# Optimization experiments

Measured on AMD Instinct MI355X. Metric: run time of the kernel, lower is better.

Reference implementation:

```python
import jax, jax.numpy as jnp
import numpy as np

N_NODES = 50000
N_EDGES = 800000
NEG_SLOPE = 0.2  # PyG GATConv default negative_slope


def setup_inputs() -> dict:
    key = jax.random.key(0)
    ks = jax.random.split(key, 10)
    d_in, hid, heads = 128, 32, 8

    def glorot(k, shape):
        fan_in, fan_out = shape[0], shape[-1]
        s = jnp.sqrt(2.0 / (fan_in + fan_out)).astype(jnp.float32)
        return jax.random.normal(k, shape, jnp.float32) * s

    return {
        "x": jax.random.normal(ks[0], (N_NODES, d_in), jnp.float32),
        "edge_index": jax.random.randint(ks[1], (2, N_EDGES), 0, N_NODES),
        "W1": glorot(ks[2], (d_in, heads * hid)),
        "a1_src": glorot(ks[3], (heads, hid)),
        "a1_dst": glorot(ks[4], (heads, hid)),
        "b1": jnp.zeros((heads * hid,), jnp.float32),
        "W2": glorot(ks[5], (heads * hid, hid)),
        "a2_src": glorot(ks[6], (1, hid)),
        "a2_dst": glorot(ks[7], (1, hid)),
        "b2": jnp.zeros((hid,), jnp.float32),
    }


def _gat_layer(x, src, dst, W, a_src, a_dst, b, concat):
    # PyG GATConv: h = x @ W, split into heads; alpha_e = softmax_over_dst(
    #   leaky_relu(<h[src], a_src> + <h[dst], a_dst>)); out = scatter-sum alpha*h[src].
    N = x.shape[0]
    H, D = a_src.shape
    h = (x @ W).reshape(N, H, D)                      # [N, H, D]
    score_s = jnp.einsum("nhd,hd->nh", h, a_src)      # [N, H]
    score_d = jnp.einsum("nhd,hd->nh", h, a_dst)
    e = jax.nn.leaky_relu(score_s[src] + score_d[dst], NEG_SLOPE)  # [E, H]
    # numerically-stable softmax over incoming edges per destination node
    m = jax.ops.segment_max(e, dst, num_segments=N)
    ex = jnp.exp(e - m[dst])
    denom = jax.ops.segment_sum(ex, dst, num_segments=N)
    alpha = ex / (denom[dst] + 1e-16)                 # [E, H]
    out = jax.ops.segment_sum(alpha[:, :, None] * h[src], dst, num_segments=N)  # [N, H, D]
    out = out.reshape(N, H * D) if concat else out[:, 0]
    return out + b


def reference(x, edge_index, W1, a1_src, a1_dst, b1, W2, a2_src, a2_dst, b2):
    N = x.shape[0]
    # PyG GATConv add_self_loops=True
    loop = jnp.arange(N, dtype=edge_index.dtype)
    src = jnp.concatenate([edge_index[0], loop])
    dst = jnp.concatenate([edge_index[1], loop])
    h = _gat_layer(x, src, dst, W1, a1_src, a1_dst, b1, concat=True)
    h = jax.nn.relu(h)
    # dropout(p=0.4) is identity in eval mode (deterministic reference)
    return _gat_layer(h, src, dst, W2, a2_src, a2_dst, b2, concat=False)
```

## Files before the change

### kernel.cpp

```cpp
#include <hip/hip_runtime.h>
#include <hip/hip_fp16.h>
#include <math.h>

#define N_NODES 50000
#define N_EDGES 800000
#define E_TOT (N_EDGES + N_NODES)
#define N_RT 3125
#define CAP 64

typedef unsigned int uint;
typedef unsigned short ushort;
typedef float f32x4 __attribute__((ext_vector_type(4)));
typedef short v8s __attribute__((ext_vector_type(8)));

__device__ __forceinline__ ushort f2bf(float f) {
    uint u = __float_as_uint(f);
    return (ushort)((u + 0x7FFFu + ((u >> 16) & 1u)) >> 16);
}
__device__ __forceinline__ float bf2f(ushort u) {
    return __uint_as_float((uint)u << 16);
}
__device__ __forceinline__ float bflo(uint v) { return __uint_as_float(v << 16); }
__device__ __forceinline__ float bfhi(uint v) { return __uint_as_float(v & 0xFFFF0000u); }

__device__ __forceinline__ int kmap(int g, int j) {
    return ((j >> 2) << 4) + (g << 2) + (j & 3);
}


__global__ void wprep_k(const float* __restrict__ W1, const float* __restrict__ a1s,
                        const float* __restrict__ a1d, const float* __restrict__ W2,
                        ushort* __restrict__ W1f, ushort* __restrict__ W2b,
                        ushort* __restrict__ W2r, ushort* __restrict__ Abf,
                        ushort* __restrict__ Arf, int* __restrict__ cnt) {
    for (int i = blockIdx.x * 256 + threadIdx.x; i < N_NODES; i += 21 * 256)
        cnt[i] = 0;

    if (blockIdx.x < 16) {
        int idx = blockIdx.x * 256 + threadIdx.x;
        int lane = idx & 63, ks = (idx >> 6) & 3, ct = idx >> 8;
        int g = lane >> 4, col = ct * 16 + (lane & 15);
        ushort us[8];
        #pragma unroll
        for (int j = 0; j < 8; j++) {
            int k = ks * 32 + kmap(g, j);
            us[j] = f2bf(W1[(size_t)k * 256 + col]);
        }
        uint4 pk;
        pk.x = (uint)us[0] | ((uint)us[1] << 16);
        pk.y = (uint)us[2] | ((uint)us[3] << 16);
        pk.z = (uint)us[4] | ((uint)us[5] << 16);
        pk.w = (uint)us[6] | ((uint)us[7] << 16);
        *((uint4*)(W1f + ((size_t)(ct * 4 + ks) * 64 + lane) * 8)) = pk;
    } else if (blockIdx.x < 20) {
        int idx = (blockIdx.x - 16) * 256 + threadIdx.x;
        int lane = idx & 63, ks = (idx >> 6) & 7, ct = idx >> 9;
        int g = lane >> 4, col = ct * 16 + (lane & 15);
        ushort ub[8], ur[8];
        #pragma unroll
        for (int j = 0; j < 8; j++) {
            int k = ks * 32 + kmap(g, j);
            float v = W2[(size_t)k * 32 + col];
            ub[j] = f2bf(v);
            ur[j] = f2bf(v - bf2f(ub[j]));
        }
        uint4 pb, pr;
        pb.x = (uint)ub[0] | ((uint)ub[1] << 16);
        pb.y = (uint)ub[2] | ((uint)ub[3] << 16);
        pb.z = (uint)ub[4] | ((uint)ub[5] << 16);
        pb.w = (uint)ub[6] | ((uint)ub[7] << 16);
        pr.x = (uint)ur[0] | ((uint)ur[1] << 16);
        pr.y = (uint)ur[2] | ((uint)ur[3] << 16);
        pr.z = (uint)ur[4] | ((uint)ur[5] << 16);
        pr.w = (uint)ur[6] | ((uint)ur[7] << 16);
        *((uint4*)(W2b + ((size_t)(ct * 8 + ks) * 64 + lane) * 8)) = pb;
        *((uint4*)(W2r + ((size_t)(ct * 8 + ks) * 64 + lane) * 8)) = pr;
    } else if (blockIdx.x == 20) {
        int t = threadIdx.x;
        int lane = t & 63, ks = t >> 6;
        int jcol = lane & 15, g = lane >> 4;
        int hh = (jcol < 8) ? jcol : jcol - 8;
        const float* a = (jcol < 8) ? (a1s + hh * 32) : (a1d + hh * 32);
        ushort ub[8], ur[8];
        #pragma unroll
        for (int j = 0; j < 8; j++) {
            int k = ks * 32 + kmap(g, j);
            const float* wrow = W1 + (size_t)k * 256 + hh * 32;
            float v = 0.f;
            #pragma unroll 8
            for (int d = 0; d < 32; d++) v = fmaf(wrow[d], a[d], v);
            ub[j] = f2bf(v);
            ur[j] = f2bf(v - bf2f(ub[j]));
        }
        uint4 pb, pr;
        pb.x = (uint)ub[0] | ((uint)ub[1] << 16);
        pb.y = (uint)ub[2] | ((uint)ub[3] << 16);
        pb.z = (uint)ub[4] | ((uint)ub[5] << 16);
        pb.w = (uint)ub[6] | ((uint)ub[7] << 16);
        pr.x = (uint)ur[0] | ((uint)ur[1] << 16);
        pr.y = (uint)ur[2] | ((uint)ur[3] << 16);
        pr.z = (uint)ur[4] | ((uint)ur[5] << 16);
        pr.w = (uint)ur[6] | ((uint)ur[7] << 16);
        *((uint4*)(Abf + ((size_t)ks * 64 + lane) * 8)) = pb;
        *((uint4*)(Arf + ((size_t)ks * 64 + lane) * 8)) = pr;
    }
}


__global__ __launch_bounds__(256) void scat_k(const int* __restrict__ ei,
                                              int* __restrict__ cnt,
                                              ushort* __restrict__ csr) {
    int t = blockIdx.x * 256 + threadIdx.x;
    if (t < N_EDGES / 8) {
        int4 sv0 = ((const int4*)ei)[2 * t];
        int4 sv1 = ((const int4*)ei)[2 * t + 1];
        int4 dv0 = ((const int4*)(ei + N_EDGES))[2 * t];
        int4 dv1 = ((const int4*)(ei + N_EDGES))[2 * t + 1];
        int p0 = atomicAdd(&cnt[dv0.x], 1);
        int p1 = atomicAdd(&cnt[dv0.y], 1);
        int p2 = atomicAdd(&cnt[dv0.z], 1);
        int p3 = atomicAdd(&cnt[dv0.w], 1);
        int p4 = atomicAdd(&cnt[dv1.x], 1);
        int p5 = atomicAdd(&cnt[dv1.y], 1);
        int p6 = atomicAdd(&cnt[dv1.z], 1);
        int p7 = atomicAdd(&cnt[dv1.w], 1);
        if (p0 < CAP) csr[dv0.x * CAP + p0] = (ushort)sv0.x;
        if (p1 < CAP) csr[dv0.y * CAP + p1] = (ushort)sv0.y;
        if (p2 < CAP) csr[dv0.z * CAP + p2] = (ushort)sv0.z;
        if (p3 < CAP) csr[dv0.w * CAP + p3] = (ushort)sv0.w;
        if (p4 < CAP) csr[dv1.x * CAP + p4] = (ushort)sv1.x;
        if (p5 < CAP) csr[dv1.y * CAP + p5] = (ushort)sv1.y;
        if (p6 < CAP) csr[dv1.z * CAP + p6] = (ushort)sv1.z;
        if (p7 < CAP) csr[dv1.w * CAP + p7] = (ushort)sv1.w;
    } else if (t < N_EDGES / 8 + (N_NODES + 3) / 4) {
        int n0 = (t - N_EDGES / 8) * 4;
        int p[4];
        #pragma unroll
        for (int j = 0; j < 4; j++) {
            int n = n0 + j;
            p[j] = (n < N_NODES) ? atomicAdd(&cnt[n], 1) : CAP;
        }
        #pragma unroll
        for (int j = 0; j < 4; j++) {
            int n = n0 + j;
            if (n < N_NODES && p[j] < CAP) csr[n * CAP + p[j]] = (ushort)n;
        }
    }
}


__global__ __launch_bounds__(256) void fgemm1_k(
        const float* __restrict__ x, const ushort* __restrict__ W1f,
        const ushort* __restrict__ Abf, const ushort* __restrict__ Arf,
        ushort* __restrict__ h1u, float* __restrict__ s1s,
        float* __restrict__ s1d) {
    int lane = threadIdx.x & 63, wv = threadIdx.x >> 6;
    int rt = blockIdx.x * 2 + (wv >> 1);
    int half = wv & 1;
    if (rt >= N_RT) return;
    int r = lane & 15, g = lane >> 4;
    const float* xrow = x + ((size_t)rt * 16 + r) * 128;

    v8s xb[4], xr[4];
    #pragma unroll
    for (int ks = 0; ks < 4; ks++) {
        float4 fa = *((const float4*)(xrow + ks * 32 + g * 4));
        float4 fb = *((const float4*)(xrow + ks * 32 + 16 + g * 4));
        ushort b0 = f2bf(fa.x), b1 = f2bf(fa.y), b2 = f2bf(fa.z), b3 = f2bf(fa.w);
        ushort b4 = f2bf(fb.x), b5 = f2bf(fb.y), b6 = f2bf(fb.z), b7 = f2bf(fb.w);
        uint4 p;
        p.x = (uint)b0 | ((uint)b1 << 16);
        p.y = (uint)b2 | ((uint)b3 << 16);
        p.z = (uint)b4 | ((uint)b5 << 16);
        p.w = (uint)b6 | ((uint)b7 << 16);
        xb[ks] = *((v8s*)&p);
        if (half == 0) {
            ushort r0 = f2bf(fa.x - bf2f(b0)), r1 = f2bf(fa.y - bf2f(b1));
            ushort r2 = f2bf(fa.z - bf2f(b2)), r3 = f2bf(fa.w - bf2f(b3));
            ushort r4 = f2bf(fb.x - bf2f(b4)), r5 = f2bf(fb.y - bf2f(b5));
            ushort r6 = f2bf(fb.z - bf2f(b6)), r7 = f2bf(fb.w - bf2f(b7));
            uint4 q;
            q.x = (uint)r0 | ((uint)r1 << 16);
            q.y = (uint)r2 | ((uint)r3 << 16);
            q.z = (uint)r4 | ((uint)r5 << 16);
            q.w = (uint)r6 | ((uint)r7 << 16);
            xr[ks] = *((v8s*)&q);
        }
    }

    if (half == 0) {
        f32x4 sacc = (f32x4){0.f, 0.f, 0.f, 0.f};
        const v8s* abp = (const v8s*)Abf;
        const v8s* arp = (const v8s*)Arf;
        #pragma unroll
        for (int ks = 0; ks < 4; ks++) {
            v8s ab = abp[ks * 64 + lane];
            v8s ar = arp[ks * 64 + lane];
            sacc = __builtin_amdgcn_mfma_f32_16x16x32_bf16(ab, xb[ks], sacc, 0, 0, 0);
            sacc = __builtin_amdgcn_mfma_f32_16x16x32_bf16(ar, xb[ks], sacc, 0, 0, 0);
            sacc = __builtin_amdgcn_mfma_f32_16x16x32_bf16(ab, xr[ks], sacc, 0, 0, 0);
        }
        int row = rt * 16 + r;
        float4 sv;
        sv.x = sacc[0]; sv.y = sacc[1]; sv.z = sacc[2]; sv.w = sacc[3];
        if (g < 2) *((float4*)(s1s + (size_t)row * 8 + g * 4)) = sv;
        else       *((float4*)(s1d + (size_t)row * 8 + (g - 2) * 4)) = sv;
    }

    f32x4 acc[8];
    #pragma unroll
    for (int c = 0; c < 8; c++) acc[c] = (f32x4){0.f, 0.f, 0.f, 0.f};
    const v8s* bp = (const v8s*)W1f + (size_t)half * 8 * 4 * 64;
    #pragma unroll
    for (int ks = 0; ks < 4; ks++) {
        #pragma unroll
        for (int c = 0; c < 8; c++) {
            v8s wf = bp[(c * 4 + ks) * 64 + lane];
            acc[c] = __builtin_amdgcn_mfma_f32_16x16x32_bf16(wf, xb[ks], acc[c], 0, 0, 0);
        }
    }

    ushort* hrow = h1u + ((size_t)rt * 16 + r) * 256 + half * 128;
    #pragma unroll
    for (int c = 0; c < 8; c++) {
        uint lo = (uint)f2bf(acc[c][0]) | ((uint)f2bf(acc[c][1]) << 16);
        uint hi = (uint)f2bf(acc[c][2]) | ((uint)f2bf(acc[c][3]) << 16);
        *((uint2*)(hrow + c * 16 + g * 4)) = make_uint2(lo, hi);
    }
}


__global__ __launch_bounds__(256) void agg1g_k(
        const ushort* __restrict__ csr, const int* __restrict__ cnt,
        const ushort* __restrict__ h1u, const float* __restrict__ s1s,
        const float* __restrict__ s1d, const float* __restrict__ b1,
        const ushort* __restrict__ W2b, const ushort* __restrict__ W2r,
        const float* __restrict__ a2s, const float* __restrict__ a2d,
        ushort* __restrict__ h2u, float* __restrict__ s2s,
        float* __restrict__ s2d) {
    __shared__ float els[4][CAP][8];
    __shared__ ushort hrt[16][264];
    int lane = threadIdx.x & 63;
    int wv = threadIdx.x >> 6;
    int base = blockIdx.x * 16;
    int e8 = lane >> 3, h8 = lane & 7;
    int hB = lane >> 3;
    int c0 = 4 * lane;
    float4 bv = *((const float4*)(b1 + c0));
    const uint2* hv = (const uint2*)h1u;

    for (int q = 0; q < 4; q++) {
        int row = wv * 4 + q;
        int n = base + row;
        int beg = n * CAP;
        int deg = min(cnt[n], CAP);
        int end = beg + deg;

        float sd = s1d[n * 8 + h8];
        float m = -3.4e38f, d = 0.f;
        for (int i = beg + e8; i < end; i += 8) {
            int s = csr[i];
            float e = s1s[s * 8 + h8] + sd;
            e = (e >= 0.f) ? e : 0.2f * e;
            els[wv][i - beg][h8] = e;
            float mn = fmaxf(m, e);
            d = d * __expf(m - mn) + __expf(e - mn);
            m = mn;
        }
        #pragma unroll
        for (int mask = 8; mask <= 32; mask <<= 1) {
            float om = __shfl_xor(m, mask);
            float od = __shfl_xor(d, mask);
            float nm = fmaxf(m, om);
            d = d * __expf(m - nm) + od * __expf(om - nm);
            m = nm;
        }
        float inv = 1.f / (d + 1e-16f);
        float mB = __shfl(m, hB);
        float invB = __shfl(inv, hB);

        const float* ep = &els[wv][0][hB];
        float acc0 = 0.f, acc1 = 0.f, acc2 = 0.f, acc3 = 0.f;
        int j = 0;
        for (; j + 3 < deg; j += 4) {
            uint2 cs = *((const uint2*)(csr + beg + j));
            int s0 = cs.x & 0xFFFF, s1 = cs.x >> 16;
            int s2 = cs.y & 0xFFFF, s3 = cs.y >> 16;
            float p0 = __expf(ep[(j + 0) * 8] - mB);
            float p1 = __expf(ep[(j + 1) * 8] - mB);
            float p2 = __expf(ep[(j + 2) * 8] - mB);
            float p3 = __expf(ep[(j + 3) * 8] - mB);
            uint2 v0 = hv[(size_t)s0 * 64 + lane];
            uint2 v1 = hv[(size_t)s1 * 64 + lane];
            uint2 v2 = hv[(size_t)s2 * 64 + lane];
            uint2 v3 = hv[(size_t)s3 * 64 + lane];
            acc0 = fmaf(p0, bflo(v0.x), acc0);
            acc1 = fmaf(p0, bfhi(v0.x), acc1);
            acc2 = fmaf(p0, bflo(v0.y), acc2);
            acc3 = fmaf(p0, bfhi(v0.y), acc3);
            acc0 = fmaf(p1, bflo(v1.x), acc0);
            acc1 = fmaf(p1, bfhi(v1.x), acc1);
            acc2 = fmaf(p1, bflo(v1.y), acc2);
            acc3 = fmaf(p1, bfhi(v1.y), acc3);
            acc0 = fmaf(p2, bflo(v2.x), acc0);
            acc1 = fmaf(p2, bfhi(v2.x), acc1);
            acc2 = fmaf(p2, bflo(v2.y), acc2);
            acc3 = fmaf(p2, bfhi(v2.y), acc3);
            acc0 = fmaf(p3, bflo(v3.x), acc0);
            acc1 = fmaf(p3, bfhi(v3.x), acc1);
            acc2 = fmaf(p3, bflo(v3.y), acc2);
            acc3 = fmaf(p3, bfhi(v3.y), acc3);
        }
        for (; j < deg; j++) {
            int s0 = csr[beg + j];
            float p0 = __expf(ep[j * 8] - mB);
            uint2 v0 = hv[(size_t)s0 * 64 + lane];
            acc0 = fmaf(p0, bflo(v0.x), acc0);
            acc1 = fmaf(p0, bfhi(v0.x), acc1);
            acc2 = fmaf(p0, bflo(v0.y), acc2);
            acc3 = fmaf(p0, bfhi(v0.y), acc3);
        }
        float o0 = fmaxf(fmaf(acc0, invB, bv.x), 0.f);
        float o1 = fmaxf(fmaf(acc1, invB, bv.y), 0.f);
        float o2 = fmaxf(fmaf(acc2, invB, bv.z), 0.f);
        float o3 = fmaxf(fmaf(acc3, invB, bv.w), 0.f);
        uint lo = (uint)f2bf(o0) | ((uint)f2bf(o1) << 16);
        uint hi = (uint)f2bf(o2) | ((uint)f2bf(o3) << 16);
        *((uint2*)&hrt[row][c0]) = make_uint2(lo, hi);
    }
    __syncthreads();

    if (threadIdx.x < 64) {
        int r = lane & 15, g = lane >> 4;
        int row = base + r;
        v8s af[8];
        #pragma unroll
        for (int ks = 0; ks < 8; ks++) {
            uint2 u0 = *((const uint2*)&hrt[r][ks * 32 + g * 4]);
            uint2 u1 = *((const uint2*)&hrt[r][ks * 32 + 16 + g * 4]);
            uint4 p; p.x = u0.x; p.y = u0.y; p.z = u1.x; p.w = u1.y;
            af[ks] = *((v8s*)&p);
        }
        f32x4 acc[2];
        acc[0] = (f32x4){0.f, 0.f, 0.f, 0.f};
        acc[1] = (f32x4){0.f, 0.f, 0.f, 0.f};
        const v8s* wbp = (const v8s*)W2b;
        const v8s* wrp = (const v8s*)W2r;
        #pragma unroll
        for (int ks = 0; ks < 8; ks++) {
            #pragma unroll
            for (int ct = 0; ct < 2; ct++) {
                v8s wb = wbp[(ct * 8 + ks) * 64 + lane];
                v8s wr = wrp[(ct * 8 + ks) * 64 + lane];
                acc[ct] = __builtin_amdgcn_mfma_f32_16x16x32_bf16(wb, af[ks], acc[ct], 0, 0, 0);
                acc[ct] = __builtin_amdgcn_mfma_f32_16x16x32_bf16(wr, af[ks], acc[ct], 0, 0, 0);
            }
        }
        float ps = 0.f, pd = 0.f;
        #pragma unroll
        for (int ct = 0; ct < 2; ct++) {
            #pragma unroll
            for (int qq = 0; qq < 4; qq++) {
                int c = ct * 16 + g * 4 + qq;
                ps = fmaf(acc[ct][qq], a2s[c], ps);
                pd = fmaf(acc[ct][qq], a2d[c], pd);
            }
        }
        ps += __shfl_xor(ps, 16); ps += __shfl_xor(ps, 32);
        pd += __shfl_xor(pd, 16); pd += __shfl_xor(pd, 32);
        if (g == 0) { s2s[row] = ps; s2d[row] = pd; }
        #pragma unroll
        for (int ct = 0; ct < 2; ct++) {
            uint lo = (uint)f2bf(acc[ct][0]) | ((uint)f2bf(acc[ct][1]) << 16);
            uint hi = (uint)f2bf(acc[ct][2]) | ((uint)f2bf(acc[ct][3]) << 16);
            *((uint2*)(h2u + (size_t)row * 32 + ct * 16 + g * 4)) = make_uint2(lo, hi);
        }
    }
}


__global__ __launch_bounds__(256) void agg2_k(
        const ushort* __restrict__ csr, const int* __restrict__ cnt,
        const ushort* __restrict__ h2u, const float* __restrict__ s2s,
        const float* __restrict__ s2d, const float* __restrict__ b2,
        float* __restrict__ out) {
    int lane = threadIdx.x & 63;
    int n = blockIdx.x * 4 + (threadIdx.x >> 6);
    int beg = n * CAP;
    int end = beg + min(cnt[n], CAP);
    float sd = s2d[n];

    float m = -3.4e38f, dd = 0.f;
    for (int i = beg + lane; i < end; i += 64) {
        float e = s2s[csr[i]] + sd;
        e = (e >= 0.f) ? e : 0.2f * e;
        float mn = fmaxf(m, e);
        dd = dd * __expf(m - mn) + __expf(e - mn);
        m = mn;
    }
    #pragma unroll
    for (int mask = 1; mask <= 32; mask <<= 1) {
        float om = __shfl_xor(m, mask);
        float od = __shfl_xor(dd, mask);
        float nm = fmaxf(m, om);
        dd = dd * __expf(m - nm) + od * __expf(om - nm);
        m = nm;
    }
    float inv = 1.f / (dd + 1e-16f);

    int e4 = lane >> 4, cp = lane & 15;
    float acc0 = 0.f, acc1 = 0.f;
    for (int c0 = beg; c0 < end; c0 += 64) {
        int i = c0 + lane;
        int sL = 0; float aL = 0.f;
        if (i < end) {
            sL = csr[i];
            float e = s2s[sL] + sd;
            e = (e >= 0.f) ? e : 0.2f * e;
            aL = __expf(e - m) * inv;
        }
        int nsub = min(64, end - c0);
        for (int el = 0; el < nsub; el += 4) {
            int local = el + e4;
            int se = __shfl(sL, local);
            float ae = __shfl(aL, local);
            uint v = *((const uint*)(h2u + (size_t)se * 32 + cp * 2));
            acc0 = fmaf(ae, bflo(v), acc0);
            acc1 = fmaf(ae, bfhi(v), acc1);
        }
    }
    acc0 += __shfl_xor(acc0, 16); acc0 += __shfl_xor(acc0, 32);
    acc1 += __shfl_xor(acc1, 16); acc1 += __shfl_xor(acc1, 32);
    if (lane < 16) {
        float2 bv = ((const float2*)b2)[cp];
        float2 o; o.x = acc0 + bv.x; o.y = acc1 + bv.y;
        ((float2*)(out + (size_t)n * 32))[cp] = o;
    }
}


extern "C" void kernel_launch(void* const* d_in, const int* in_sizes, int n_in,
                              void* d_out, int out_size, void* d_ws, size_t ws_size,
                              hipStream_t stream) {
    const float* x   = (const float*)d_in[0];
    const int*   ei  = (const int*)d_in[1];
    const float* W1  = (const float*)d_in[2];
    const float* a1s = (const float*)d_in[3];
    const float* a1d = (const float*)d_in[4];
    const float* b1  = (const float*)d_in[5];
    const float* W2  = (const float*)d_in[6];
    const float* a2s = (const float*)d_in[7];
    const float* a2d = (const float*)d_in[8];
    const float* b2  = (const float*)d_in[9];
    float* out = (float*)d_out;

    char* w = (char*)d_ws;
    ushort* h1u   = (ushort*)w; w += (size_t)N_NODES * 256 * 2;
    ushort* W1f   = (ushort*)w; w += (size_t)16 * 4 * 64 * 8 * 2;
    ushort* Abf   = (ushort*)w; w += (size_t)4 * 64 * 8 * 2;
    ushort* Arf   = (ushort*)w; w += (size_t)4 * 64 * 8 * 2;
    ushort* W2b   = (ushort*)w; w += (size_t)2 * 8 * 64 * 8 * 2;
    ushort* W2r   = (ushort*)w; w += (size_t)2 * 8 * 64 * 8 * 2;
    ushort* h2u   = (ushort*)w; w += (size_t)N_NODES * 32 * 2;
    float* s1s    = (float*)w;  w += (size_t)N_NODES * 8 * 4;
    float* s1d    = (float*)w;  w += (size_t)N_NODES * 8 * 4;
    float* s2s    = (float*)w;  w += (size_t)N_NODES * 4;
    float* s2d    = (float*)w;  w += (size_t)N_NODES * 4;
    int* cnt    = (int*)w; w += (size_t)N_NODES * 4;
    ushort* csr = (ushort*)w; w += (size_t)N_NODES * CAP * 2;

    int nscat = (N_EDGES / 8 + (N_NODES + 3) / 4 + 255) / 256;

    wprep_k<<<21, 256, 0, stream>>>(W1, a1s, a1d, W2, W1f, W2b, W2r, Abf, Arf, cnt);
    scat_k<<<nscat, 256, 0, stream>>>(ei, cnt, csr);
    fgemm1_k<<<(N_RT + 1) / 2, 256, 0, stream>>>(x, W1f, Abf, Arf, h1u, s1s, s1d);
    agg1g_k<<<N_NODES / 16, 256, 0, stream>>>(csr, cnt, h1u, s1s, s1d, b1,
                                              W2b, W2r, a2s, a2d, h2u, s2s, s2d);
    agg2_k<<<N_NODES / 4, 256, 0, stream>>>(csr, cnt, h2u, s2s, s2d, b2, out);
}
```

Measured before the change: 192.1 us.

## Fuse edge scatter and first-layer GEMM into one launch; pre-seed self loops

Merges the CSR scatter kernel and the layer-1 GEMM kernel into a single launch whose blocks split by index: the first blocks scatter edges and the rest compute the GEMM tiles. The two jobs are independent, so they can overlap on the GPU, and one launch boundary disappears. Self loops are now written in the weight-prep kernel by setting each count to 1 and storing the node's own index in slot 0, so the scatter no longer does atomics for them. Self loops now always sit first in each neighbour list, which changes the summation order slightly but is otherwise equivalent.

```diff
diff --git a/kernel.cpp b/kernel.cpp
--- a/kernel.cpp
+++ b/kernel.cpp
@@ -7,6 +7,7 @@
 #define E_TOT (N_EDGES + N_NODES)
 #define N_RT 3125
 #define CAP 64
+#define NBLK_SCAT ((N_EDGES / 8 + 255) / 256)
 
 typedef unsigned int uint;
 typedef unsigned short ushort;
@@ -32,9 +33,12 @@
                         const float* __restrict__ a1d, const float* __restrict__ W2,
                         ushort* __restrict__ W1f, ushort* __restrict__ W2b,
                         ushort* __restrict__ W2r, ushort* __restrict__ Abf,
-                        ushort* __restrict__ Arf, int* __restrict__ cnt) {
-    for (int i = blockIdx.x * 256 + threadIdx.x; i < N_NODES; i += 21 * 256)
-        cnt[i] = 0;
+                        ushort* __restrict__ Arf, int* __restrict__ cnt,
+                        ushort* __restrict__ csr) {
+    for (int i = blockIdx.x * 256 + threadIdx.x; i < N_NODES; i += 21 * 256) {
+        cnt[i] = 1;
+        csr[(size_t)i * CAP] = (ushort)i;
+    }
 
     if (blockIdx.x < 16) {
         int idx = blockIdx.x * 256 + threadIdx.x;
@@ -107,11 +111,16 @@
 }
 
 
-__global__ __launch_bounds__(256) void scat_k(const int* __restrict__ ei,
-                                              int* __restrict__ cnt,
-                                              ushort* __restrict__ csr) {
-    int t = blockIdx.x * 256 + threadIdx.x;
-    if (t < N_EDGES / 8) {
+__global__ __launch_bounds__(256) void fsg_k(
+        const int* __restrict__ ei, int* __restrict__ cnt,
+        ushort* __restrict__ csr,
+        const float* __restrict__ x, const ushort* __restrict__ W1f,
+        const ushort* __restrict__ Abf, const ushort* __restrict__ Arf,
+        ushort* __restrict__ h1u, float* __restrict__ s1s,
+        float* __restrict__ s1d) {
+    if (blockIdx.x < NBLK_SCAT) {
+        int t = blockIdx.x * 256 + threadIdx.x;
+        if (t >= N_EDGES / 8) return;
         int4 sv0 = ((const int4*)ei)[2 * t];
         int4 sv1 = ((const int4*)ei)[2 * t + 1];
         int4 dv0 = ((const int4*)(ei + N_EDGES))[2 * t];
@@ -132,30 +141,11 @@
         if (p5 < CAP) csr[dv1.y * CAP + p5] = (ushort)sv1.y;
         if (p6 < CAP) csr[dv1.z * CAP + p6] = (ushort)sv1.z;
         if (p7 < CAP) csr[dv1.w * CAP + p7] = (ushort)sv1.w;
-    } else if (t < N_EDGES / 8 + (N_NODES + 3) / 4) {
-        int n0 = (t - N_EDGES / 8) * 4;
-        int p[4];
-        #pragma unroll
-        for (int j = 0; j < 4; j++) {
-            int n = n0 + j;
-            p[j] = (n < N_NODES) ? atomicAdd(&cnt[n], 1) : CAP;
-        }
-        #pragma unroll
-        for (int j = 0; j < 4; j++) {
-            int n = n0 + j;
-            if (n < N_NODES && p[j] < CAP) csr[n * CAP + p[j]] = (ushort)n;
-        }
-    }
-}
-
-
-__global__ __launch_bounds__(256) void fgemm1_k(
-        const float* __restrict__ x, const ushort* __restrict__ W1f,
-        const ushort* __restrict__ Abf, const ushort* __restrict__ Arf,
-        ushort* __restrict__ h1u, float* __restrict__ s1s,
-        float* __restrict__ s1d) {
+        return;
+    }
+
     int lane = threadIdx.x & 63, wv = threadIdx.x >> 6;
-    int rt = blockIdx.x * 2 + (wv >> 1);
+    int rt = (blockIdx.x - NBLK_SCAT) * 2 + (wv >> 1);
     int half = wv & 1;
     if (rt >= N_RT) return;
     int r = lane & 15, g = lane >> 4;
@@ -469,11 +459,10 @@
     int* cnt    = (int*)w; w += (size_t)N_NODES * 4;
     ushort* csr = (ushort*)w; w += (size_t)N_NODES * CAP * 2;
 
-    int nscat = (N_EDGES / 8 + (N_NODES + 3) / 4 + 255) / 256;
-
-    wprep_k<<<21, 256, 0, stream>>>(W1, a1s, a1d, W2, W1f, W2b, W2r, Abf, Arf, cnt);
-    scat_k<<<nscat, 256, 0, stream>>>(ei, cnt, csr);
-    fgemm1_k<<<(N_RT + 1) / 2, 256, 0, stream>>>(x, W1f, Abf, Arf, h1u, s1s, s1d);
+    wprep_k<<<21, 256, 0, stream>>>(W1, a1s, a1d, W2, W1f, W2b, W2r, Abf, Arf,
+                                    cnt, csr);
+    fsg_k<<<NBLK_SCAT + (N_RT + 1) / 2, 256, 0, stream>>>(
+        ei, cnt, csr, x, W1f, Abf, Arf, h1u, s1s, s1d);
     agg1g_k<<<N_NODES / 16, 256, 0, stream>>>(csr, cnt, h1u, s1s, s1d, b1,
                                               W2b, W2r, a2s, a2d, h2u, s2s, s2d);
     agg2_k<<<N_NODES / 4, 256, 0, stream>>>(csr, cnt, h2u, s2s, s2d, b2, out);
```

Measured after the change: 183.8 us, median of 2. 1.05x faster.
